# Kernel tuning notes

Measured on AMD Instinct MI355X. Metric: run time of the kernel, lower is better.

## Reference

```python
import jax, jax.numpy as jnp
import numpy as np
from jax import lax

B, IN_C, OUT_C, K, Z_DIM, H, W = 32, 128, 128, 3, 64, 96, 96
PAD = K // 2


def setup_inputs() -> dict:
    key = jax.random.key(0)
    k1, k2, k3, k4, k5, k6 = jax.random.split(key, 6)
    fan = (2.0 / (IN_C * K * K)) ** 0.5
    x = jax.random.normal(k1, (B, IN_C, H, W), dtype=jnp.float32)
    z = jax.random.normal(k2, (B, Z_DIM), dtype=jnp.float32)
    base_weight = jax.random.normal(k3, (OUT_C, IN_C, K, K), dtype=jnp.float32) * fan
    # torch nn.Linear weights are [out_features, in_features]
    gate_weight = jax.random.normal(k4, (OUT_C, Z_DIM), dtype=jnp.float32) * (1.0 / Z_DIM ** 0.5)
    pw_weight = jax.random.normal(k5, (OUT_C * IN_C, Z_DIM), dtype=jnp.float32) * (1.0 / Z_DIM ** 0.5)
    dw_weight = jax.random.normal(k6, (OUT_C * K * K, Z_DIM), dtype=jnp.float32) * (1.0 / Z_DIM ** 0.5)
    return {"x": x, "z": z, "base_weight": base_weight, "gate_weight": gate_weight,
            "pw_weight": pw_weight, "dw_weight": dw_weight}


def _merged_weight(z, base_weight, gate_weight, pw_weight, dw_weight):
    # BaseOp.get_weight: base * gate(z)  -> [B, out_c, in_c, k, k]
    gate = z @ gate_weight.T                       # [B, out_c]
    w_base = base_weight[None] * gate[:, :, None, None, None]
    # PWOp.get_weight (groups=1): [B, out_c, in_c, 1, 1]
    pw = (z @ pw_weight.T).reshape(B, OUT_C, IN_C)
    # DWOp.get_weight: [B, out_c, 1, k, k]
    dw = (z @ dw_weight.T).reshape(B, OUT_C, 1, K, K)
    # delta = pw * dw broadcast -> [B, out_c, in_c, k, k]
    delta = pw[:, :, :, None, None] * dw
    return w_base + delta


def _per_sample_conv(xi, wi):
    # xi: [in_c, H, W], wi: [out_c, in_c, k, k]
    return lax.conv_general_dilated(
        xi[None], wi, window_strides=(1, 1),
        padding=((PAD, PAD), (PAD, PAD)),
        dimension_numbers=("NCHW", "OIHW", "NCHW"))[0]


def reference(x, z, base_weight, gate_weight, pw_weight, dw_weight):
    w = _merged_weight(z, base_weight, gate_weight, pw_weight, dw_weight)
    return jax.vmap(_per_sample_conv)(x, w)  # [B, out_c, H, W]
```

## Files before the change

### kernel.cpp

```cpp
#include <hip/hip_runtime.h>
#include <hip/hip_bf16.h>

typedef __bf16 bf16x8 __attribute__((ext_vector_type(8)));
typedef float f32x4 __attribute__((ext_vector_type(4)));

__device__ __forceinline__ int swz(int n, int k) {
  int pair = n >> 1;
  int s = (((n & 1) << 2) | k) ^ (pair & 7);
  return (pair << 7) + (s << 4);
}

__device__ __forceinline__ void load_lds16(const void* g, void* l) {
  __builtin_amdgcn_global_load_lds((const __attribute__((address_space(1))) void*)g,
                                   (__attribute__((address_space(3))) void*)l, 16, 0, 0);
}

__global__ __launch_bounds__(512) void prep_x_kernel(const float* __restrict__ x,
                                                     __hip_bfloat16* __restrict__ xn) {
  __shared__ float tile[128][97];
  int h = blockIdx.x;
  int b = blockIdx.y;
  const float* src = x + (size_t)b * 128 * 9216 + h * 96;
  for (int f = threadIdx.x; f < 3072; f += 512) {
    int ic = f / 24, w4 = f - ic * 24;
    float4 v = *(const float4*)(src + (size_t)ic * 9216 + w4 * 4);
    tile[ic][w4 * 4 + 0] = v.x; tile[ic][w4 * 4 + 1] = v.y;
    tile[ic][w4 * 4 + 2] = v.z; tile[ic][w4 * 4 + 3] = v.w;
  }
  __syncthreads();
  __hip_bfloat16* bb  = xn + (size_t)b * 4 * 307328;
  __hip_bfloat16* dst = bb + (h + 1) * 3136 + 32;
  for (int o = threadIdx.x; o < 1536; o += 512) {
    int grp = o / 384, rem = o - grp * 384;
    int w = rem >> 2, chunk = rem & 3;
    __hip_bfloat16 tmp[8];
    #pragma unroll
    for (int e = 0; e < 8; e++) tmp[e] = __float2bfloat16(tile[grp * 32 + chunk * 8 + e][w]);
    *(uint4*)(dst + (size_t)grp * 307328 + w * 32 + chunk * 8) = *(uint4*)tmp;
  }
  if (threadIdx.x < 32) {
    int u = threadIdx.x;
    int grp = u >> 3, rem = u & 7;
    int pw = (rem >> 2) ? 97 : 0, k = rem & 3;
    *(uint4*)(bb + (size_t)grp * 307328 + ((h + 1) * 98 + pw) * 32 + k * 8) = make_uint4(0, 0, 0, 0);
  }
  if (h == 0 || h == 95) {
    int ph = (h == 0) ? 0 : 97;
    for (int u = threadIdx.x; u < 1568; u += 512) {
      int grp = u / 392, rem = u - grp * 392;
      int pw = rem >> 2, k = rem & 3;
      *(uint4*)(bb + (size_t)grp * 307328 + (ph * 98 + pw) * 32 + k * 8) = make_uint4(0, 0, 0, 0);
    }
  }
}

__global__ __launch_bounds__(256) void prep_w_kernel(
    const float* __restrict__ z, const float* __restrict__ gw,
    const float* __restrict__ pww, const float* __restrict__ dww,
    const float* __restrict__ base, __hip_bfloat16* __restrict__ Wt) {
  __shared__ float zs[2048];
  __shared__ float res[138][33];
  int oc = blockIdx.x;
  for (int i = threadIdx.x; i < 2048; i += 256) zs[i] = z[i];
  __syncthreads();
  int row = threadIdx.x;
  if (row < 138) {
    const float* wrow = (row == 0) ? gw + (size_t)oc * 64
                      : (row < 10) ? dww + ((size_t)oc * 9 + (row - 1)) * 64
                                   : pww + ((size_t)oc * 128 + (row - 10)) * 64;
    float wr[64];
    #pragma unroll
    for (int i = 0; i < 16; i++) {
      float4 v = ((const float4*)wrow)[i];
      wr[4*i] = v.x; wr[4*i+1] = v.y; wr[4*i+2] = v.z; wr[4*i+3] = v.w;
    }
    for (int b = 0; b < 32; b++) {
      float a = 0.f;
      #pragma unroll
      for (int i = 0; i < 64; i++) a += zs[b * 64 + i] * wr[i];
      res[row][b] = a;
    }
  }
  __syncthreads();
  for (int e = threadIdx.x; e < 18432; e += 256) {
    int icp = e & 15;
    int r1 = e >> 4;
    int tap = r1 % 9, bg = r1 / 9;
    int grp = bg & 3, b = bg >> 2;
    int ic = grp * 32 + icp * 2;
    float g = res[0][b], d = res[1 + tap][b];
    float p0 = res[10 + ic][b], p1 = res[11 + ic][b];
    const float* bp = base + ((size_t)(oc * 128 + ic)) * 9 + tap;
    __hip_bfloat162 o2 = {__float2bfloat16(bp[0] * g + p0 * d),
                          __float2bfloat16(bp[9] * g + p1 * d)};
    *(__hip_bfloat162*)(Wt + (((size_t)bg * 9 + tap) * 128 + oc) * 32 + icp * 2) = o2;
  }
}

__global__ __launch_bounds__(256, 2) void conv_kernel(
    const __hip_bfloat16* __restrict__ xn, const __hip_bfloat16* __restrict__ Wt,
    float* __restrict__ out) {
  __shared__ __align__(16) char smem[73728];
  char* const xb0 = smem;
  char* const xb1 = smem + 24576;
  char* const wb0 = smem + 49152;
  char* const wb1 = smem + 61440;

  int bid = blockIdx.x;
  int X = bid & 7, q = bid >> 3;
  int logical = X * 288 + q;
  int b   = logical / 72;
  int rem = logical - b * 72;
  int ocg = rem & 1;
  int t36 = rem >> 1;
  int hr  = t36 / 3;
  int wc  = t36 - hr * 3;
  int h0 = hr * 8, w0 = wc * 32;

  int tid = threadIdx.x;
  int lane = tid & 63, wid = tid >> 6;
  int l15 = lane & 15, lk = lane >> 4;

  int xoff[6];
  #pragma unroll
  for (int j = 0; j < 6; j++) {
    int p = j * 256 + tid; if (p > 1359) p = 1359;
    int pair = p >> 3, v = (p & 7) ^ (pair & 7);
    int n = (pair << 1) | (v >> 2), k = v & 3;
    int hh = n / 34, ww = n - hh * 34;
    xoff[j] = ((h0 + hh) * 98 + (w0 + ww)) * 32 + k * 8;
  }
  int wsoff[3];
  #pragma unroll
  for (int i = 0; i < 3; i++) {
    int p = i * 256 + tid;
    int pair = p >> 3, v = (p & 7) ^ (pair & 7);
    int n = (pair << 1) | (v >> 2), k = v & 3;
    int dx = n >> 6, ocl = n & 63;
    wsoff[i] = (dx * 128 + ocg * 64 + ocl) * 32 + k * 8;
  }

  const __hip_bfloat16* xbase = xn + (size_t)b * 4 * 307328;
  const __hip_bfloat16* wbase = Wt + (size_t)b * 147456;

  f32x4 acc[4][4];
  #pragma unroll
  for (int i = 0; i < 4; i++)
    #pragma unroll
    for (int j = 0; j < 4; j++) acc[i][j] = (f32x4){0.f, 0.f, 0.f, 0.f};

  #pragma unroll
  for (int j = 0; j < 6; j++)
    load_lds16(xbase + xoff[j], xb0 + ((j * 256 + wid * 64) << 4));
  #pragma unroll
  for (int i = 0; i < 3; i++)
    load_lds16(wbase + wsoff[i], wb0 + ((i * 256 + wid * 64) << 4));

#define PHASE(G, T, XCUR, XNXT, WCUR, WNXT, DOX, DOW, VM)                          \
  {                                                                                \
    __builtin_amdgcn_s_barrier();                                                  \
    if (DOW) {                                                                     \
      const __hip_bfloat16* wsrc = wbase + (size_t)((G) * 9 + (T) * 3 + 3) * 4096; \
      _Pragma("unroll")                                                            \
      for (int i = 0; i < 3; i++)                                                  \
        load_lds16(wsrc + wsoff[i], (WNXT) + ((i * 256 + wid * 64) << 4));         \
    }                                                                              \
    if (DOX) {                                                                     \
      const __hip_bfloat16* xsrc = xbase + (size_t)((G) + 1) * 307328;             \
      _Pragma("unroll")                                                            \
      for (int j = 0; j < 6; j++)                                                  \
        load_lds16(xsrc + xoff[j], (XNXT) + ((j * 256 + wid * 64) << 4));          \
    }                                                                              \
    asm volatile("s_waitcnt vmcnt(" #VM ")" ::: "memory");                         \
    __builtin_amdgcn_s_barrier();                                                  \
    _Pragma("unroll")                                                              \
    for (int dx = 0; dx < 3; dx++) {                                               \
      bf16x8 bfr[4], afr[4];                                                       \
      _Pragma("unroll")                                                            \
      for (int j = 0; j < 4; j++)                                                  \
        bfr[j] = *(const bf16x8*)((WCUR) + swz(dx * 64 + j * 16 + l15, lk));       \
      _Pragma("unroll")                                                            \
      for (int i = 0; i < 4; i++) {                                                \
        int r = wid * 2 + (i >> 1) + (T);                                          \
        int c = ((i & 1) << 4) + l15 + dx;                                         \
        afr[i] = *(const bf16x8*)((XCUR) + swz(r * 34 + c, lk));                   \
      }                                                                            \
      __builtin_amdgcn_s_setprio(1);                                               \
      _Pragma("unroll")                                                            \
      for (int i = 0; i < 4; i++)                                                  \
        _Pragma("unroll")                                                          \
        for (int j = 0; j < 4; j++)                                                \
          acc[i][j] = __builtin_amdgcn_mfma_f32_16x16x32_bf16(afr[i], bfr[j],      \
                                                              acc[i][j], 0, 0, 0); \
      __builtin_amdgcn_s_setprio(0);                                               \
    }                                                                              \
  }

  PHASE(0, 0, xb0, xb1, wb0, wb1, 1, 1, 9)
  PHASE(0, 1, xb0, xb1, wb1, wb0, 0, 1, 9)
  PHASE(0, 2, xb0, xb1, wb0, wb1, 0, 1, 3)
  PHASE(1, 0, xb1, xb0, wb1, wb0, 1, 1, 9)
  PHASE(1, 1, xb1, xb0, wb0, wb1, 0, 1, 9)
  PHASE(1, 2, xb1, xb0, wb1, wb0, 0, 1, 3)
  PHASE(2, 0, xb0, xb1, wb0, wb1, 1, 1, 9)
  PHASE(2, 1, xb0, xb1, wb1, wb0, 0, 1, 9)
  PHASE(2, 2, xb0, xb1, wb0, wb1, 0, 1, 3)
  PHASE(3, 0, xb1, xb0, wb1, wb0, 0, 1, 3)
  PHASE(3, 1, xb1, xb0, wb0, wb1, 0, 1, 3)
  PHASE(3, 2, xb1, xb0, wb1, wb0, 0, 0, 0)
#undef PHASE

  float* ob = out + ((size_t)b * 128 + ocg * 64) * 9216;
  #pragma unroll
  for (int j = 0; j < 4; j++) {
    int oc = j * 16 + l15;
    float* op = ob + (size_t)oc * 9216 + h0 * 96 + w0 + lk * 4;
    #pragma unroll
    for (int i = 0; i < 4; i++) {
      int m0 = wid * 64 + i * 16;
      *(f32x4*)(op + (m0 >> 5) * 96 + (m0 & 31)) = acc[i][j];
    }
  }
}

extern "C" void kernel_launch(void* const* d_in, const int* in_sizes, int n_in,
                              void* d_out, int out_size, void* d_ws, size_t ws_size,
                              hipStream_t stream) {
  const float* x   = (const float*)d_in[0];
  const float* z   = (const float*)d_in[1];
  const float* bw  = (const float*)d_in[2];
  const float* gw  = (const float*)d_in[3];
  const float* pww = (const float*)d_in[4];
  const float* dww = (const float*)d_in[5];
  float* out = (float*)d_out;

  char* ws = (char*)d_ws;
  __hip_bfloat16* xn = (__hip_bfloat16*)ws;
  __hip_bfloat16* Wt = (__hip_bfloat16*)(ws + 78675968);

  hipLaunchKernelGGL(prep_x_kernel, dim3(96, 32), dim3(512), 0, stream, x, xn);
  hipLaunchKernelGGL(prep_w_kernel, dim3(128), dim3(256), 0, stream,
                     z, gw, pww, dww, bw, Wt);
  hipLaunchKernelGGL(conv_kernel,   dim3(2304), dim3(256), 0, stream, xn, Wt, out);
}
```

Before: 166.5 us.

## Single-buffer the input tile to fit three blocks per CU

The conv kernel drops its double-buffered input tile in favour of one LDS buffer, cutting shared memory from 72KB to 48KB and raising launch bounds to three blocks per CU. Each new input-channel group is loaded at the start of its phase and waited on before compute, so input loads no longer overlap MFMA work within a block. The bet is that the extra resident block hides that latency, at the cost of exposed load waits and tighter register limits.

```diff
diff --git a/kernel.cpp b/kernel.cpp
--- a/kernel.cpp
+++ b/kernel.cpp
@@ -97,14 +97,13 @@
   }
 }
 
-__global__ __launch_bounds__(256, 2) void conv_kernel(
+__global__ __launch_bounds__(256, 3) void conv_kernel(
     const __hip_bfloat16* __restrict__ xn, const __hip_bfloat16* __restrict__ Wt,
     float* __restrict__ out) {
-  __shared__ __align__(16) char smem[73728];
-  char* const xb0 = smem;
-  char* const xb1 = smem + 24576;
-  char* const wb0 = smem + 49152;
-  char* const wb1 = smem + 61440;
+  __shared__ __align__(16) char smem[49152];
+  char* const xt  = smem;
+  char* const wb0 = smem + 24576;
+  char* const wb1 = smem + 36864;
 
   int bid = blockIdx.x;
   int X = bid & 7, q = bid >> 3;
@@ -150,26 +149,26 @@
     for (int j = 0; j < 4; j++) acc[i][j] = (f32x4){0.f, 0.f, 0.f, 0.f};
 
   #pragma unroll
-  for (int j = 0; j < 6; j++)
-    load_lds16(xbase + xoff[j], xb0 + ((j * 256 + wid * 64) << 4));
-  #pragma unroll
   for (int i = 0; i < 3; i++)
     load_lds16(wbase + wsoff[i], wb0 + ((i * 256 + wid * 64) << 4));
-
-#define PHASE(G, T, XCUR, XNXT, WCUR, WNXT, DOX, DOW, VM)                          \
+  #pragma unroll
+  for (int j = 0; j < 6; j++)
+    load_lds16(xbase + xoff[j], xt + ((j * 256 + wid * 64) << 4));
+
+#define PHASE(G, T, WCUR, WNXT, DOX, DOW, VM)                                      \
   {                                                                                \
     __builtin_amdgcn_s_barrier();                                                  \
+    if (DOX) {                                                                     \
+      const __hip_bfloat16* xsrc = xbase + (size_t)(G) * 307328;                   \
+      _Pragma("unroll")                                                            \
+      for (int j = 0; j < 6; j++)                                                  \
+        load_lds16(xsrc + xoff[j], xt + ((j * 256 + wid * 64) << 4));              \
+    }                                                                              \
     if (DOW) {                                                                     \
       const __hip_bfloat16* wsrc = wbase + (size_t)((G) * 9 + (T) * 3 + 3) * 4096; \
       _Pragma("unroll")                                                            \
       for (int i = 0; i < 3; i++)                                                  \
         load_lds16(wsrc + wsoff[i], (WNXT) + ((i * 256 + wid * 64) << 4));         \
-    }                                                                              \
-    if (DOX) {                                                                     \
-      const __hip_bfloat16* xsrc = xbase + (size_t)((G) + 1) * 307328;             \
-      _Pragma("unroll")                                                            \
-      for (int j = 0; j < 6; j++)                                                  \
-        load_lds16(xsrc + xoff[j], (XNXT) + ((j * 256 + wid * 64) << 4));          \
     }                                                                              \
     asm volatile("s_waitcnt vmcnt(" #VM ")" ::: "memory");                         \
     __builtin_amdgcn_s_barrier();                                                  \
@@ -183,7 +182,7 @@
       for (int i = 0; i < 4; i++) {                                                \
         int r = wid * 2 + (i >> 1) + (T);                                          \
         int c = ((i & 1) << 4) + l15 + dx;                                         \
-        afr[i] = *(const bf16x8*)((XCUR) + swz(r * 34 + c, lk));                   \
+        afr[i] = *(const bf16x8*)(xt + swz(r * 34 + c, lk));                       \
       }                                                                            \
       __builtin_amdgcn_s_setprio(1);                                               \
       _Pragma("unroll")                                                            \
@@ -196,18 +195,18 @@
     }                                                                              \
   }
 
-  PHASE(0, 0, xb0, xb1, wb0, wb1, 1, 1, 9)
-  PHASE(0, 1, xb0, xb1, wb1, wb0, 0, 1, 9)
-  PHASE(0, 2, xb0, xb1, wb0, wb1, 0, 1, 3)
-  PHASE(1, 0, xb1, xb0, wb1, wb0, 1, 1, 9)
-  PHASE(1, 1, xb1, xb0, wb0, wb1, 0, 1, 9)
-  PHASE(1, 2, xb1, xb0, wb1, wb0, 0, 1, 3)
-  PHASE(2, 0, xb0, xb1, wb0, wb1, 1, 1, 9)
-  PHASE(2, 1, xb0, xb1, wb1, wb0, 0, 1, 9)
-  PHASE(2, 2, xb0, xb1, wb0, wb1, 0, 1, 3)
-  PHASE(3, 0, xb1, xb0, wb1, wb0, 0, 1, 3)
-  PHASE(3, 1, xb1, xb0, wb0, wb1, 0, 1, 3)
-  PHASE(3, 2, xb1, xb0, wb1, wb0, 0, 0, 0)
+  PHASE(0, 0, wb0, wb1, 0, 1, 3)
+  PHASE(0, 1, wb1, wb0, 0, 1, 3)
+  PHASE(0, 2, wb0, wb1, 0, 1, 3)
+  PHASE(1, 0, wb1, wb0, 1, 1, 3)
+  PHASE(1, 1, wb0, wb1, 0, 1, 3)
+  PHASE(1, 2, wb1, wb0, 0, 1, 3)
+  PHASE(2, 0, wb0, wb1, 1, 1, 3)
+  PHASE(2, 1, wb1, wb0, 0, 1, 3)
+  PHASE(2, 2, wb0, wb1, 0, 1, 3)
+  PHASE(3, 0, wb1, wb0, 1, 1, 3)
+  PHASE(3, 1, wb0, wb1, 0, 1, 3)
+  PHASE(3, 2, wb1, wb0, 0, 0, 0)
 #undef PHASE
 
   float* ob = out + ((size_t)b * 128 + ocg * 64) * 9216;
```

New measurement: 161.6 us. 2.9% less time.
